# Kernel tuning notes

Measured on AMD Instinct MI355X. Metric: run time of the kernel, lower is better.

## Reference

```python
import jax, jax.numpy as jnp
import numpy as np

N = 50000      # nodes
E = 800000     # edges (before self-loops)
IN = 128       # in_channels
HID = 64       # hidden_channels
HEADS = 2
OUT = 128      # out_channels
NEG_SLOPE = 0.2


def setup_inputs() -> dict:
    key = jax.random.key(0)
    ks = jax.random.split(key, 12)
    p = lambda k, shape: jax.random.normal(k, shape, dtype=jnp.float32) * 0.05
    return {
        "x": jax.random.normal(ks[0], (N, IN), dtype=jnp.float32),
        "edge_index": jax.random.randint(ks[1], (2, E), 0, N, dtype=jnp.int32),
        "W1": p(ks[2], (IN, HEADS * HID)),
        "a_src1": p(ks[3], (HEADS, HID)),
        "a_dst1": p(ks[4], (HEADS, HID)),
        "b1": jnp.zeros((HEADS * HID,), dtype=jnp.float32),
        "W2": p(ks[5], (HEADS * HID, OUT)),
        "a_src2": p(ks[6], (1, OUT)),
        "a_dst2": p(ks[7], (1, OUT)),
        "b2": jnp.zeros((OUT,), dtype=jnp.float32),
    }


def _gat_conv(x, src, dst, W, a_src, a_dst, b, heads, out_c, concat):
    n = x.shape[0]
    h = (x @ W).reshape(n, heads, out_c)                # [N,H,C]
    al_s = jnp.sum(h * a_src, axis=-1)                  # [N,H]
    al_d = jnp.sum(h * a_dst, axis=-1)                  # [N,H]
    e = jax.nn.leaky_relu(al_s[src] + al_d[dst], NEG_SLOPE)  # [E',H]
    # softmax over edges grouped by destination node (numerically stable)
    e_max = jax.ops.segment_max(e, dst, num_segments=n)
    ee = jnp.exp(e - e_max[dst])
    denom = jax.ops.segment_sum(ee, dst, num_segments=n)
    alpha = ee / (denom[dst] + 1e-16)                   # [E',H]
    out = jax.ops.segment_sum(alpha[:, :, None] * h[src], dst, num_segments=n)  # [N,H,C]
    out = out.reshape(n, heads * out_c) if concat else out.mean(axis=1)
    return out + b


def reference(x, edge_index, W1, a_src1, a_dst1, b1, W2, a_src2, a_dst2, b2):
    n = x.shape[0]
    loops = jnp.arange(n, dtype=edge_index.dtype)       # PyG GATConv adds self-loops
    src = jnp.concatenate([edge_index[0], loops])
    dst = jnp.concatenate([edge_index[1], loops])
    h = jax.nn.elu(_gat_conv(x, src, dst, W1, a_src1, a_dst1, b1, HEADS, HID, True))
    return _gat_conv(h, src, dst, W2, a_src2, a_dst2, b2, 1, OUT, False)
```

## Files before the change

### kernel.cpp

```cpp
#include <hip/hip_runtime.h>
#include <hip/hip_bf16.h>
#include <math.h>

#define N_NODES 50000
#define N_EDGES 800000
#define NEG_SLOPE 0.2f
#define NBUCK ((N_NODES + 255) / 256)
#define CCHUNK 4096
#define DCAP 8192

__device__ inline float lrelu(float x) { return fmaxf(x, NEG_SLOPE * x); }

__device__ inline unsigned bf16rne(float f) {
    unsigned u = __float_as_uint(f);
    return (u + 0x7fffu + ((u >> 16) & 1u)) >> 16;
}

__global__ __launch_bounds__(256) void bucketcount_kernel(const int* __restrict__ ei,
                                                          int* __restrict__ gbcnt) {
    __shared__ int lc[NBUCK];
    for (int i = threadIdx.x; i < NBUCK; i += 256) lc[i] = 0;
    __syncthreads();
    int stride = gridDim.x * 256;
    for (int e = blockIdx.x * 256 + threadIdx.x; e < N_EDGES; e += stride)
        atomicAdd(&lc[ei[N_EDGES + e] >> 8], 1);
    __syncthreads();
    for (int i = threadIdx.x; i < NBUCK; i += 256)
        if (lc[i]) atomicAdd(&gbcnt[i], lc[i]);
}

__global__ __launch_bounds__(256) void bucketscan_kernel(const int* __restrict__ gbcnt,
                                                         int* __restrict__ bbase,
                                                         int* __restrict__ bcur) {
    __shared__ int ss[256];
    int t = threadIdx.x;
    int v = (t < NBUCK) ? gbcnt[t] : 0;
    ss[t] = v;
    __syncthreads();
    for (int d = 1; d < 256; d <<= 1) {
        int u = (t >= d) ? ss[t - d] : 0;
        __syncthreads();
        ss[t] += u;
        __syncthreads();
    }
    int excl = ss[t] - v;
    if (t < NBUCK) { bbase[t] = excl; bcur[t] = excl; }
    if (t == 0) bbase[NBUCK] = N_EDGES;
}

__global__ __launch_bounds__(256) void bucketscatter_kernel(const int* __restrict__ ei,
                                                            int* __restrict__ bcur,
                                                            int2* __restrict__ bpairs) {
    __shared__ int cnt[NBUCK], startl[NBUCK], baseg[NBUCK], cur2[NBUCK];
    __shared__ int ss[256];
    __shared__ int2 stage[CCHUNK];
    int t = threadIdx.x;
    int e0 = blockIdx.x * CCHUNK;
    int nume = min(CCHUNK, N_EDGES - e0);
    for (int i = t; i < NBUCK; i += 256) { cnt[i] = 0; cur2[i] = 0; }
    __syncthreads();
    int src[CCHUNK / 256], dst[CCHUNK / 256];
    #pragma unroll
    for (int j = 0; j < CCHUNK / 256; ++j) {
        int idx = t + j * 256;
        if (idx < nume) {
            src[j] = ei[e0 + idx];
            dst[j] = ei[N_EDGES + e0 + idx];
            atomicAdd(&cnt[dst[j] >> 8], 1);
        } else dst[j] = -1;
    }
    __syncthreads();
    {
        int v = (t < NBUCK) ? cnt[t] : 0;
        ss[t] = v;
        __syncthreads();
        for (int d = 1; d < 256; d <<= 1) {
            int u = (t >= d) ? ss[t - d] : 0;
            __syncthreads();
            ss[t] += u;
            __syncthreads();
        }
        if (t < NBUCK) startl[t] = ss[t] - v;
    }
    __syncthreads();
    if (t < NBUCK && cnt[t] > 0) baseg[t] = atomicAdd(&bcur[t], cnt[t]);
    __syncthreads();
    #pragma unroll
    for (int j = 0; j < CCHUNK / 256; ++j) {
        if (dst[j] >= 0) {
            int b = dst[j] >> 8;
            int slot = startl[b] + atomicAdd(&cur2[b], 1);
            stage[slot] = make_int2(src[j], dst[j]);
        }
    }
    __syncthreads();
    for (int i = t; i < nume; i += 256) {
        int2 p = stage[i];
        int b = p.y >> 8;
        bpairs[baseg[b] + (i - startl[b])] = p;
    }
}

__global__ __launch_bounds__(256) void csrfinalize_kernel(const int2* __restrict__ bpairs,
                                                          const int* __restrict__ bbase,
                                                          int* __restrict__ ptr,
                                                          int* __restrict__ csr) {
    __shared__ int cnt[256], excl[256], cur[256];
    __shared__ int ss[256];
    __shared__ int2 P[DCAP];
    int b = blockIdx.x, t = threadIdx.x;
    int bb = bbase[b], be = bbase[b + 1];
    int n = be - bb;
    int d0 = b << 8;
    int dmax = min(256, N_NODES - d0);
    bool fits = (n <= DCAP);
    cnt[t] = 0; cur[t] = 0;
    __syncthreads();
    for (int i = t; i < n; i += 256) {
        int2 p = bpairs[bb + i];
        if (fits) P[i] = p;
        atomicAdd(&cnt[p.y & 255], 1);
    }
    __syncthreads();
    {
        int v = cnt[t];
        ss[t] = v;
        __syncthreads();
        for (int d = 1; d < 256; d <<= 1) {
            int u = (t >= d) ? ss[t - d] : 0;
            __syncthreads();
            ss[t] += u;
            __syncthreads();
        }
        excl[t] = ss[t] - v;
    }
    __syncthreads();
    if (t < dmax) ptr[d0 + t] = bb + excl[t];
    if (b == NBUCK - 1 && t == 0) ptr[N_NODES] = N_EDGES;
    for (int i = t; i < n; i += 256) {
        int2 p = fits ? P[i] : bpairs[bb + i];
        int ld = p.y & 255;
        int pos = bb + excl[ld] + atomicAdd(&cur[ld], 1);
        csr[pos] = p.x;
    }
}

#define GB_ROWS 64
template <int H>
__global__ __launch_bounds__(256) void gemm_kernel(const float* __restrict__ X,
                                                   const float* __restrict__ W,
                                                   const float* __restrict__ asrc,
                                                   const float* __restrict__ adst,
                                                   unsigned short* __restrict__ Hb,
                                                   float* __restrict__ als,
                                                   float* __restrict__ ald,
                                                   int nrows) {
    __shared__ float xt[GB_ROWS][132];
    const int tid = threadIdx.x;
    const int r0 = blockIdx.x * GB_ROWS;
    #pragma unroll
    for (int i = 0; i < 8; ++i) {
        int idx = tid + 256 * i;
        int r = idx >> 5, c4 = (idx & 31) * 4;
        int gr = r0 + r;
        float4 v = make_float4(0.f, 0.f, 0.f, 0.f);
        if (gr < nrows) v = *(const float4*)(X + (size_t)gr * 128 + c4);
        *(float4*)(&xt[r][c4]) = v;
    }
    __syncthreads();
    const int c0 = (tid & 31) * 4;
    const int rbase = (tid >> 5) * 8;
    const int q = tid & 31;
    float acc[8][4];
    #pragma unroll
    for (int i = 0; i < 8; ++i)
        #pragma unroll
        for (int j = 0; j < 4; ++j) acc[i][j] = 0.f;
    #pragma unroll 4
    for (int k = 0; k < 128; ++k) {
        float4 w4 = *(const float4*)(W + k * 128 + c0);
        float xv[8];
        #pragma unroll
        for (int i = 0; i < 8; ++i) xv[i] = xt[rbase + i][k];
        #pragma unroll
        for (int i = 0; i < 8; ++i) {
            acc[i][0] = fmaf(xv[i], w4.x, acc[i][0]);
            acc[i][1] = fmaf(xv[i], w4.y, acc[i][1]);
            acc[i][2] = fmaf(xv[i], w4.z, acc[i][2]);
            acc[i][3] = fmaf(xv[i], w4.w, acc[i][3]);
        }
    }
    float4 as4 = *(const float4*)(asrc + c0);
    float4 ad4 = *(const float4*)(adst + c0);
    #pragma unroll
    for (int i = 0; i < 8; ++i) {
        int gr = r0 + rbase + i;
        bool ok = gr < nrows;
        if (ok) {
            uint2 p;
            p.x = bf16rne(acc[i][0]) | (bf16rne(acc[i][1]) << 16);
            p.y = bf16rne(acc[i][2]) | (bf16rne(acc[i][3]) << 16);
            *(uint2*)(Hb + (size_t)gr * 128 + c0) = p;
        }
        float sp = acc[i][0] * as4.x + acc[i][1] * as4.y + acc[i][2] * as4.z + acc[i][3] * as4.w;
        float dp = acc[i][0] * ad4.x + acc[i][1] * ad4.y + acc[i][2] * ad4.z + acc[i][3] * ad4.w;
        #pragma unroll
        for (int off = 1; off < (H == 2 ? 16 : 32); off <<= 1) {
            sp += __shfl_xor(sp, off);
            dp += __shfl_xor(dp, off);
        }
        if (ok) {
            if (H == 2) {
                if (q == 0)  { als[(size_t)gr * 2]     = sp; ald[(size_t)gr * 2]     = dp; }
                if (q == 16) { als[(size_t)gr * 2 + 1] = sp; ald[(size_t)gr * 2 + 1] = dp; }
            } else {
                if (q == 0) { als[gr] = sp; ald[gr] = dp; }
            }
        }
    }
}

template <int H, int DO_ELU>
__global__ __launch_bounds__(256) void aggregate_kernel(const unsigned short* __restrict__ Hb,
                                                        const float* __restrict__ als,
                                                        const float* __restrict__ aldv,
                                                        const int* __restrict__ ptr,
                                                        const int* __restrict__ csr,
                                                        const float* __restrict__ bias,
                                                        float* __restrict__ out) {
    __shared__ int   s_src[4][64];
    __shared__ float s_p[4][H][64];
    const int w = threadIdx.x >> 6;
    const int lane = threadIdx.x & 63;
    const int d = blockIdx.x * 4 + w;
    if (d >= N_NODES) return;
    const int head = (H == 2) ? (lane >> 5) : 0;

    int beg = ptr[d], end = ptr[d + 1];

    float ald0, ald1 = 0.f, es0, es1 = 0.f;
    if (H == 2) {
        float2 ta = *(const float2*)(aldv + (size_t)d * 2);
        float2 ts = *(const float2*)(als + (size_t)d * 2);
        ald0 = ta.x; ald1 = ta.y;
        es0 = lrelu(ts.x + ald0); es1 = lrelu(ts.y + ald1);
    } else {
        ald0 = aldv[d]; es0 = lrelu(als[d] + ald0);
    }

    int k0 = beg + lane;
    int src0 = 0;
    float e0 = -INFINITY, e1 = -INFINITY;
    if (k0 < end) {
        src0 = csr[k0];
        if (H == 2) {
            float2 t = *(const float2*)(als + (size_t)src0 * 2);
            e0 = lrelu(t.x + ald0); e1 = lrelu(t.y + ald1);
        } else e0 = lrelu(als[src0] + ald0);
    }
    float m0 = fmaxf(es0, e0);
    float m1 = (H == 2) ? fmaxf(es1, e1) : 0.f;
    for (int k = k0 + 64; k < end; k += 64) {
        int s = csr[k];
        if (H == 2) {
            float2 t = *(const float2*)(als + (size_t)s * 2);
            m0 = fmaxf(m0, lrelu(t.x + ald0));
            m1 = fmaxf(m1, lrelu(t.y + ald1));
        } else m0 = fmaxf(m0, lrelu(als[s] + ald0));
    }
    #pragma unroll
    for (int off = 32; off; off >>= 1) {
        m0 = fmaxf(m0, __shfl_xor(m0, off));
        if (H == 2) m1 = fmaxf(m1, __shfl_xor(m1, off));
    }

    float l0 = 0.f, l1 = 0.f;
    float ax0 = 0.f, ay0 = 0.f, ax1 = 0.f, ay1 = 0.f;
    float ax2 = 0.f, ay2 = 0.f, ax3 = 0.f, ay3 = 0.f;

    for (int t0 = beg; t0 < end; t0 += 64) {
        int cnt = min(64, end - t0);
        int k = t0 + lane;
        if (k < end) {
            int s; float f0, f1 = 0.f;
            if (t0 == beg) { s = src0; f0 = e0; f1 = e1; }
            else {
                s = csr[k];
                if (H == 2) {
                    float2 t = *(const float2*)(als + (size_t)s * 2);
                    f0 = lrelu(t.x + ald0); f1 = lrelu(t.y + ald1);
                } else f0 = lrelu(als[s] + ald0);
            }
            float p0 = __expf(f0 - m0);
            l0 += p0;
            s_src[w][lane] = s;
            s_p[w][0][lane] = p0;
            if (H == 2) {
                float p1 = __expf(f1 - m1);
                l1 += p1;
                s_p[w][1][lane] = p1;
            }
        }
        int j = 0;
        for (; j + 3 < cnt; j += 4) {
            int sA = s_src[w][j],     sB = s_src[w][j + 1];
            int sC = s_src[w][j + 2], sD = s_src[w][j + 3];
            float pA = s_p[w][head][j],     pB = s_p[w][head][j + 1];
            float pC = s_p[w][head][j + 2], pD = s_p[w][head][j + 3];
            unsigned uA = ((const unsigned*)(Hb + (size_t)sA * 128))[lane];
            unsigned uB = ((const unsigned*)(Hb + (size_t)sB * 128))[lane];
            unsigned uC = ((const unsigned*)(Hb + (size_t)sC * 128))[lane];
            unsigned uD = ((const unsigned*)(Hb + (size_t)sD * 128))[lane];
            ax0 = fmaf(pA, __uint_as_float(uA << 16), ax0);
            ay0 = fmaf(pA, __uint_as_float(uA & 0xffff0000u), ay0);
            ax1 = fmaf(pB, __uint_as_float(uB << 16), ax1);
            ay1 = fmaf(pB, __uint_as_float(uB & 0xffff0000u), ay1);
            ax2 = fmaf(pC, __uint_as_float(uC << 16), ax2);
            ay2 = fmaf(pC, __uint_as_float(uC & 0xffff0000u), ay2);
            ax3 = fmaf(pD, __uint_as_float(uD << 16), ax3);
            ay3 = fmaf(pD, __uint_as_float(uD & 0xffff0000u), ay3);
        }
        for (; j < cnt; ++j) {
            int sA = s_src[w][j];
            float pA = s_p[w][head][j];
            unsigned uA = ((const unsigned*)(Hb + (size_t)sA * 128))[lane];
            ax0 = fmaf(pA, __uint_as_float(uA << 16), ax0);
            ay0 = fmaf(pA, __uint_as_float(uA & 0xffff0000u), ay0);
        }
    }

    float ax = (ax0 + ax1) + (ax2 + ax3);
    float ay = (ay0 + ay1) + (ay2 + ay3);
    float mh  = (head == 0) ? m0 : m1;
    float esh = (head == 0) ? es0 : es1;
    float psh = __expf(esh - mh);
    {
        unsigned u = ((const unsigned*)(Hb + (size_t)d * 128))[lane];
        ax = fmaf(psh, __uint_as_float(u << 16), ax);
        ay = fmaf(psh, __uint_as_float(u & 0xffff0000u), ay);
    }
    #pragma unroll
    for (int off = 32; off; off >>= 1) {
        l0 += __shfl_xor(l0, off);
        if (H == 2) l1 += __shfl_xor(l1, off);
    }
    float denom = ((head == 0) ? l0 : l1) + psh;
    float inv = 1.f / (denom + 1e-16f);
    float o0 = ax * inv + bias[2 * lane];
    float o1 = ay * inv + bias[2 * lane + 1];
    if (DO_ELU) {
        o0 = o0 > 0.f ? o0 : expm1f(o0);
        o1 = o1 > 0.f ? o1 : expm1f(o1);
    }
    ((float2*)(out + (size_t)d * 128))[lane] = make_float2(o0, o1);
}

extern "C" void kernel_launch(void* const* d_in, const int* in_sizes, int n_in,
                              void* d_out, int out_size, void* d_ws, size_t ws_size,
                              hipStream_t stream) {
    const float* x      = (const float*)d_in[0];
    const int*   ei     = (const int*)d_in[1];
    const float* W1     = (const float*)d_in[2];
    const float* a_src1 = (const float*)d_in[3];
    const float* a_dst1 = (const float*)d_in[4];
    const float* b1     = (const float*)d_in[5];
    const float* W2     = (const float*)d_in[6];
    const float* a_src2 = (const float*)d_in[7];
    const float* a_dst2 = (const float*)d_in[8];
    const float* b2     = (const float*)d_in[9];
    float* out = (float*)d_out;

    char* ws = (char*)d_ws;
    size_t off = 0;
    auto alloc = [&](size_t bytes) { void* p = ws + off; off += (bytes + 255) & ~(size_t)255; return p; };
    int*   ptr    = (int*)alloc((N_NODES + 1) * sizeof(int));
    int*   gbcnt  = (int*)alloc(NBUCK * sizeof(int));
    int*   bbase  = (int*)alloc((NBUCK + 1) * sizeof(int));
    int*   bcur   = (int*)alloc(NBUCK * sizeof(int));
    int2*  bpairs = (int2*)alloc((size_t)N_EDGES * sizeof(int2));
    int*   csr    = (int*)alloc(N_EDGES * sizeof(int));
    float* x2     = (float*)alloc((size_t)N_NODES * 128 * sizeof(float));
    unsigned short* hb = (unsigned short*)alloc((size_t)N_NODES * 128 * sizeof(unsigned short));
    float* als    = (float*)alloc(N_NODES * 2 * sizeof(float));
    float* ald    = (float*)alloc(N_NODES * 2 * sizeof(float));

    hipMemsetAsync(gbcnt, 0, NBUCK * sizeof(int), stream);
    bucketcount_kernel<<<256, 256, 0, stream>>>(ei, gbcnt);
    bucketscan_kernel<<<1, 256, 0, stream>>>(gbcnt, bbase, bcur);
    bucketscatter_kernel<<<(N_EDGES + CCHUNK - 1) / CCHUNK, 256, 0, stream>>>(ei, bcur, bpairs);
    csrfinalize_kernel<<<NBUCK, 256, 0, stream>>>(bpairs, bbase, ptr, csr);

    int gblocks = (N_NODES + GB_ROWS - 1) / GB_ROWS;
    int wblocks = (N_NODES + 3) / 4;

    gemm_kernel<2><<<gblocks, 256, 0, stream>>>(x, W1, a_src1, a_dst1, hb, als, ald, N_NODES);
    aggregate_kernel<2, 1><<<wblocks, 256, 0, stream>>>(hb, als, ald, ptr, csr, b1, x2);

    gemm_kernel<1><<<gblocks, 256, 0, stream>>>(x2, W2, a_src2, a_dst2, hb, als, ald, N_NODES);
    aggregate_kernel<1, 0><<<wblocks, 256, 0, stream>>>(hb, als, ald, ptr, csr, b2, out);
}
```

Measured before the change: 191.8 us.

## Replace FP32 FMA GEMMs with split-bf16 MFMA GEMMs

```diff
diff --git a/kernel.cpp b/kernel.cpp
--- a/kernel.cpp
+++ b/kernel.cpp
@@ -3,6 +3,7 @@
 #include <math.h>
 
 #define N_NODES 50000
+#define NPAD 50048
 #define N_EDGES 800000
 #define NEG_SLOPE 0.2f
 #define NBUCK ((N_NODES + 255) / 256)
@@ -14,6 +15,12 @@
 __device__ inline unsigned bf16rne(float f) {
     unsigned u = __float_as_uint(f);
     return (u + 0x7fffu + ((u >> 16) & 1u)) >> 16;
+}
+__device__ inline float bf2f(unsigned h) { return __uint_as_float(h << 16); }
+
+__global__ void zerobuf_kernel(int* __restrict__ p) {
+    int i = threadIdx.x;
+    if (i < NBUCK) p[i] = 0;
 }
 
 __global__ __launch_bounds__(256) void bucketcount_kernel(const int* __restrict__ ei,
@@ -145,89 +152,151 @@
     }
 }
 
-#define GB_ROWS 64
+__global__ __launch_bounds__(256) void convx_kernel(const float* __restrict__ x,
+                                                    unsigned short* __restrict__ xh,
+                                                    unsigned short* __restrict__ xl,
+                                                    unsigned short* __restrict__ x2h,
+                                                    unsigned short* __restrict__ x2l) {
+    int q = blockIdx.x * 256 + threadIdx.x;
+    if (q >= NPAD * 128 / 4) return;
+    int e = q * 4;
+    int row = e >> 7;
+    float vv[4] = {0.f, 0.f, 0.f, 0.f};
+    if (row < N_NODES) {
+        float4 v = *(const float4*)(x + e);
+        vv[0] = v.x; vv[1] = v.y; vv[2] = v.z; vv[3] = v.w;
+    }
+    ushort4 hh, ll;
+    unsigned h0 = bf16rne(vv[0]), h1 = bf16rne(vv[1]), h2 = bf16rne(vv[2]), h3 = bf16rne(vv[3]);
+    hh.x = h0; hh.y = h1; hh.z = h2; hh.w = h3;
+    ll.x = bf16rne(vv[0] - bf2f(h0));
+    ll.y = bf16rne(vv[1] - bf2f(h1));
+    ll.z = bf16rne(vv[2] - bf2f(h2));
+    ll.w = bf16rne(vv[3] - bf2f(h3));
+    *(ushort4*)(xh + e) = hh;
+    *(ushort4*)(xl + e) = ll;
+    if (row >= N_NODES) {
+        ushort4 z = {0, 0, 0, 0};
+        *(ushort4*)(x2h + e) = z;
+        *(ushort4*)(x2l + e) = z;
+    }
+}
+
+__global__ __launch_bounds__(256) void convw_kernel(const float* __restrict__ W,
+                                                    unsigned short* __restrict__ wth,
+                                                    unsigned short* __restrict__ wtl) {
+    int idx = blockIdx.x * 256 + threadIdx.x;
+    if (idx >= 128 * 128) return;
+    int c = idx >> 7, k = idx & 127;
+    float v = W[(size_t)k * 128 + c];
+    unsigned h = bf16rne(v);
+    wth[idx] = (unsigned short)h;
+    wtl[idx] = (unsigned short)bf16rne(v - bf2f(h));
+}
+
 template <int H>
-__global__ __launch_bounds__(256) void gemm_kernel(const float* __restrict__ X,
-                                                   const float* __restrict__ W,
-                                                   const float* __restrict__ asrc,
-                                                   const float* __restrict__ adst,
-                                                   unsigned short* __restrict__ Hb,
-                                                   float* __restrict__ als,
-                                                   float* __restrict__ ald,
-                                                   int nrows) {
-    __shared__ float xt[GB_ROWS][132];
-    const int tid = threadIdx.x;
-    const int r0 = blockIdx.x * GB_ROWS;
-    #pragma unroll
-    for (int i = 0; i < 8; ++i) {
-        int idx = tid + 256 * i;
-        int r = idx >> 5, c4 = (idx & 31) * 4;
-        int gr = r0 + r;
-        float4 v = make_float4(0.f, 0.f, 0.f, 0.f);
-        if (gr < nrows) v = *(const float4*)(X + (size_t)gr * 128 + c4);
-        *(float4*)(&xt[r][c4]) = v;
-    }
-    __syncthreads();
-    const int c0 = (tid & 31) * 4;
-    const int rbase = (tid >> 5) * 8;
-    const int q = tid & 31;
-    float acc[8][4];
-    #pragma unroll
-    for (int i = 0; i < 8; ++i)
+__global__ __launch_bounds__(256) void gemm_mfma_kernel(const unsigned short* __restrict__ Ah,
+                                                        const unsigned short* __restrict__ Al,
+                                                        const unsigned short* __restrict__ Bh,
+                                                        const unsigned short* __restrict__ Bl,
+                                                        const float* __restrict__ asrc,
+                                                        const float* __restrict__ adst,
+                                                        unsigned short* __restrict__ Hb,
+                                                        float* __restrict__ als,
+                                                        float* __restrict__ ald,
+                                                        int nrows) {
+    using bf16x8 = __attribute__((ext_vector_type(8))) short;
+    using f32x4  = __attribute__((ext_vector_type(4))) float;
+    const int lane = threadIdx.x & 63;
+    const int wv = threadIdx.x >> 6;
+    const int l15 = lane & 15;
+    const int g = lane >> 4;
+    const int lk = g * 8;
+    const int rowbase = blockIdx.x * 128 + wv * 32;
+
+    f32x4 acc[2][8];
+    #pragma unroll
+    for (int rt = 0; rt < 2; ++rt)
         #pragma unroll
-        for (int j = 0; j < 4; ++j) acc[i][j] = 0.f;
-    #pragma unroll 4
-    for (int k = 0; k < 128; ++k) {
-        float4 w4 = *(const float4*)(W + k * 128 + c0);
-        float xv[8];
+        for (int ct = 0; ct < 8; ++ct) acc[rt][ct] = (f32x4){0.f, 0.f, 0.f, 0.f};
+
+    #pragma unroll
+    for (int kc = 0; kc < 4; ++kc) {
+        const int ko = kc * 32 + lk;
+        bf16x8 ah0 = *(const bf16x8*)(Ah + (size_t)(rowbase + l15) * 128 + ko);
+        bf16x8 ah1 = *(const bf16x8*)(Ah + (size_t)(rowbase + 16 + l15) * 128 + ko);
+        bf16x8 al0 = *(const bf16x8*)(Al + (size_t)(rowbase + l15) * 128 + ko);
+        bf16x8 al1 = *(const bf16x8*)(Al + (size_t)(rowbase + 16 + l15) * 128 + ko);
         #pragma unroll
-        for (int i = 0; i < 8; ++i) xv[i] = xt[rbase + i][k];
+        for (int ct = 0; ct < 8; ++ct) {
+            bf16x8 bh = *(const bf16x8*)(Bh + (size_t)(ct * 16 + l15) * 128 + ko);
+            bf16x8 bl = *(const bf16x8*)(Bl + (size_t)(ct * 16 + l15) * 128 + ko);
+            acc[0][ct] = __builtin_amdgcn_mfma_f32_16x16x32_bf16(ah0, bh, acc[0][ct], 0, 0, 0);
+            acc[0][ct] = __builtin_amdgcn_mfma_f32_16x16x32_bf16(ah0, bl, acc[0][ct], 0, 0, 0);
+            acc[0][ct] = __builtin_amdgcn_mfma_f32_16x16x32_bf16(al0, bh, acc[0][ct], 0, 0, 0);
+            acc[1][ct] = __builtin_amdgcn_mfma_f32_16x16x32_bf16(ah1, bh, acc[1][ct], 0, 0, 0);
+            acc[1][ct] = __builtin_amdgcn_mfma_f32_16x16x32_bf16(ah1, bl, acc[1][ct], 0, 0, 0);
+            acc[1][ct] = __builtin_amdgcn_mfma_f32_16x16x32_bf16(al1, bh, acc[1][ct], 0, 0, 0);
+        }
+    }
+
+    float as8[8], ad8[8];
+    #pragma unroll
+    for (int ct = 0; ct < 8; ++ct) { as8[ct] = asrc[ct * 16 + l15]; ad8[ct] = adst[ct * 16 + l15]; }
+
+    #pragma unroll
+    for (int rt = 0; rt < 2; ++rt) {
         #pragma unroll
-        for (int i = 0; i < 8; ++i) {
-            acc[i][0] = fmaf(xv[i], w4.x, acc[i][0]);
-            acc[i][1] = fmaf(xv[i], w4.y, acc[i][1]);
-            acc[i][2] = fmaf(xv[i], w4.z, acc[i][2]);
-            acc[i][3] = fmaf(xv[i], w4.w, acc[i][3]);
-        }
-    }
-    float4 as4 = *(const float4*)(asrc + c0);
-    float4 ad4 = *(const float4*)(adst + c0);
-    #pragma unroll
-    for (int i = 0; i < 8; ++i) {
-        int gr = r0 + rbase + i;
-        bool ok = gr < nrows;
-        if (ok) {
-            uint2 p;
-            p.x = bf16rne(acc[i][0]) | (bf16rne(acc[i][1]) << 16);
-            p.y = bf16rne(acc[i][2]) | (bf16rne(acc[i][3]) << 16);
-            *(uint2*)(Hb + (size_t)gr * 128 + c0) = p;
-        }
-        float sp = acc[i][0] * as4.x + acc[i][1] * as4.y + acc[i][2] * as4.z + acc[i][3] * as4.w;
-        float dp = acc[i][0] * ad4.x + acc[i][1] * ad4.y + acc[i][2] * ad4.z + acc[i][3] * ad4.w;
+        for (int ct = 0; ct < 8; ++ct) {
+            #pragma unroll
+            for (int j = 0; j < 4; ++j) {
+                int row = rowbase + rt * 16 + g * 4 + j;
+                if (row < nrows)
+                    Hb[(size_t)row * 128 + ct * 16 + l15] = (unsigned short)bf16rne(acc[rt][ct][j]);
+            }
+        }
         #pragma unroll
-        for (int off = 1; off < (H == 2 ? 16 : 32); off <<= 1) {
-            sp += __shfl_xor(sp, off);
-            dp += __shfl_xor(dp, off);
-        }
-        if (ok) {
+        for (int j = 0; j < 4; ++j) {
+            int row = rowbase + rt * 16 + g * 4 + j;
             if (H == 2) {
-                if (q == 0)  { als[(size_t)gr * 2]     = sp; ald[(size_t)gr * 2]     = dp; }
-                if (q == 16) { als[(size_t)gr * 2 + 1] = sp; ald[(size_t)gr * 2 + 1] = dp; }
+                float sp0 = 0.f, sp1 = 0.f, dp0 = 0.f, dp1 = 0.f;
+                #pragma unroll
+                for (int ct = 0; ct < 4; ++ct) { sp0 += acc[rt][ct][j] * as8[ct]; dp0 += acc[rt][ct][j] * ad8[ct]; }
+                #pragma unroll
+                for (int ct = 4; ct < 8; ++ct) { sp1 += acc[rt][ct][j] * as8[ct]; dp1 += acc[rt][ct][j] * ad8[ct]; }
+                #pragma unroll
+                for (int off = 1; off < 16; off <<= 1) {
+                    sp0 += __shfl_xor(sp0, off); sp1 += __shfl_xor(sp1, off);
+                    dp0 += __shfl_xor(dp0, off); dp1 += __shfl_xor(dp1, off);
+                }
+                if (l15 == 0 && row < nrows) {
+                    als[(size_t)row * 2]     = sp0; als[(size_t)row * 2 + 1] = sp1;
+                    ald[(size_t)row * 2]     = dp0; ald[(size_t)row * 2 + 1] = dp1;
+                }
             } else {
-                if (q == 0) { als[gr] = sp; ald[gr] = dp; }
+                float sp = 0.f, dp = 0.f;
+                #pragma unroll
+                for (int ct = 0; ct < 8; ++ct) { sp += acc[rt][ct][j] * as8[ct]; dp += acc[rt][ct][j] * ad8[ct]; }
+                #pragma unroll
+                for (int off = 1; off < 16; off <<= 1) {
+                    sp += __shfl_xor(sp, off); dp += __shfl_xor(dp, off);
+                }
+                if (l15 == 0 && row < nrows) { als[row] = sp; ald[row] = dp; }
             }
         }
     }
 }
 
-template <int H, int DO_ELU>
+template <int H, int DO_ELU, int BSPLIT>
 __global__ __launch_bounds__(256) void aggregate_kernel(const unsigned short* __restrict__ Hb,
                                                         const float* __restrict__ als,
                                                         const float* __restrict__ aldv,
                                                         const int* __restrict__ ptr,
                                                         const int* __restrict__ csr,
                                                         const float* __restrict__ bias,
-                                                        float* __restrict__ out) {
+                                                        float* __restrict__ out,
+                                                        unsigned short* __restrict__ oh,
+                                                        unsigned short* __restrict__ ol) {
     __shared__ int   s_src[4][64];
     __shared__ float s_p[4][H][64];
     const int w = threadIdx.x >> 6;
@@ -352,7 +421,15 @@
         o0 = o0 > 0.f ? o0 : expm1f(o0);
         o1 = o1 > 0.f ? o1 : expm1f(o1);
     }
-    ((float2*)(out + (size_t)d * 128))[lane] = make_float2(o0, o1);
+    if (BSPLIT) {
+        unsigned h0 = bf16rne(o0), h1 = bf16rne(o1);
+        ushort2 sh; sh.x = h0; sh.y = h1;
+        ushort2 sl; sl.x = bf16rne(o0 - bf2f(h0)); sl.y = bf16rne(o1 - bf2f(h1));
+        *(ushort2*)(oh + (size_t)d * 128 + 2 * lane) = sh;
+        *(ushort2*)(ol + (size_t)d * 128 + 2 * lane) = sl;
+    } else {
+        ((float2*)(out + (size_t)d * 128))[lane] = make_float2(o0, o1);
+    }
 }
 
 extern "C" void kernel_launch(void* const* d_in, const int* in_sizes, int n_in,
@@ -379,23 +456,34 @@
     int*   bcur   = (int*)alloc(NBUCK * sizeof(int));
     int2*  bpairs = (int2*)alloc((size_t)N_EDGES * sizeof(int2));
     int*   csr    = (int*)alloc(N_EDGES * sizeof(int));
-    float* x2     = (float*)alloc((size_t)N_NODES * 128 * sizeof(float));
-    unsigned short* hb = (unsigned short*)alloc((size_t)N_NODES * 128 * sizeof(unsigned short));
+    unsigned short* xbh = (unsigned short*)alloc((size_t)NPAD * 128 * 2);
+    unsigned short* xbl = (unsigned short*)alloc((size_t)NPAD * 128 * 2);
+    unsigned short* x2h = (unsigned short*)alloc((size_t)NPAD * 128 * 2);
+    unsigned short* x2l = (unsigned short*)alloc((size_t)NPAD * 128 * 2);
+    unsigned short* hb  = (unsigned short*)alloc((size_t)N_NODES * 128 * 2);
+    unsigned short* w1h = (unsigned short*)alloc(128 * 128 * 2);
+    unsigned short* w1l = (unsigned short*)alloc(128 * 128 * 2);
+    unsigned short* w2h = (unsigned short*)alloc(128 * 128 * 2);
+    unsigned short* w2l = (unsigned short*)alloc(128 * 128 * 2);
     float* als    = (float*)alloc(N_NODES * 2 * sizeof(float));
     float* ald    = (float*)alloc(N_NODES * 2 * sizeof(float));
 
-    hipMemsetAsync(gbcnt, 0, NBUCK * sizeof(int), stream);
+    zerobuf_kernel<<<1, 256, 0, stream>>>(gbcnt);
     bucketcount_kernel<<<256, 256, 0, stream>>>(ei, gbcnt);
     bucketscan_kernel<<<1, 256, 0, stream>>>(gbcnt, bbase, bcur);
     bucketscatter_kernel<<<(N_EDGES + CCHUNK - 1) / CCHUNK, 256, 0, stream>>>(ei, bcur, bpairs);
     csrfinalize_kernel<<<NBUCK, 256, 0, stream>>>(bpairs, bbase, ptr, csr);
 
-    int gblocks = (N_NODES + GB_ROWS - 1) / GB_ROWS;
+    convx_kernel<<<(NPAD * 128 / 4 + 255) / 256, 256, 0, stream>>>(x, xbh, xbl, x2h, x2l);
+    convw_kernel<<<64, 256, 0, stream>>>(W1, w1h, w1l);
+    convw_kernel<<<64, 256, 0, stream>>>(W2, w2h, w2l);
+
+    int gblocks = NPAD / 128;
     int wblocks = (N_NODES + 3) / 4;
 
-    gemm_kernel<2><<<gblocks, 256, 0, stream>>>(x, W1, a_src1, a_dst1, hb, als, ald, N_NODES);
-    aggregate_kernel<2, 1><<<wblocks, 256, 0, stream>>>(hb, als, ald, ptr, csr, b1, x2);
-
-    gemm_kernel<1><<<gblocks, 256, 0, stream>>>(x2, W2, a_src2, a_dst2, hb, als, ald, N_NODES);
-    aggregate_kernel<1, 0><<<wblocks, 256, 0, stream>>>(hb, als, ald, ptr, csr, b2, out);
-}
+    gemm_mfma_kernel<2><<<gblocks, 256, 0, stream>>>(xbh, xbl, w1h, w1l, a_src1, a_dst1, hb, als, ald, N_NODES);
+    aggregate_kernel<2, 1, 1><<<wblocks, 256, 0, stream>>>(hb, als, ald, ptr, csr, b1, nullptr, x2h, x2l);
+
+    gemm_mfma_kernel<1><<<gblocks, 256, 0, stream>>>(x2h, x2l, w2h, w2l, a_src2, a_dst2, hb, als, ald, N_NODES);
+    aggregate_kernel<1, 0, 0><<<wblocks, 256, 0, stream>>>(hb, als, ald, ptr, csr, b2, out, nullptr, nullptr);
+}
```

After: 185.3 us. -3.4%, faster.
